# Kernel optimization log

Measured on AMD Instinct MI355X. Metric: run time of the kernel, lower is better.

## Reference

```python
import jax, jax.numpy as jnp
import numpy as np

N_NODES, IN_F, HIDDEN, N_EDGES, N_TRAIN, N_CLASS = 50000, 64, 512, 160000, 80000, 7
BN_EPS = 1e-5

def _lin(k, fin, fout):
    return jax.random.normal(k, (fin, fout), jnp.float32) * 0.05, jnp.zeros((fout,), jnp.float32)

def setup_inputs() -> dict:
    key = jax.random.key(0)
    ks = jax.random.split(key, 12)
    x = jax.random.normal(ks[0], (N_NODES, IN_F), jnp.float32)
    edge_index = jax.random.randint(ks[1], (2, N_EDGES), 0, N_NODES, jnp.int32)
    train_edge_id = jax.random.randint(ks[2], (N_TRAIN,), 0, N_EDGES, jnp.int32)
    W1, b1 = _lin(ks[3], IN_F, HIDDEN)
    W2, b2 = _lin(ks[4], HIDDEN, HIDDEN)
    W3, b3 = _lin(ks[5], HIDDEN, HIDDEN)
    W4, b4 = _lin(ks[6], HIDDEN, HIDDEN)
    lin1_W, lin1_b = _lin(ks[7], HIDDEN, HIDDEN)
    lin2_W, lin2_b = _lin(ks[8], HIDDEN, HIDDEN)
    fc2_W, fc2_b = _lin(ks[9], HIDDEN, N_CLASS)
    ones = jnp.ones((HIDDEN,), jnp.float32); zeros = jnp.zeros((HIDDEN,), jnp.float32)
    return dict(x=x, edge_index=edge_index, train_edge_id=train_edge_id,
                W1=W1, b1=b1, W2=W2, b2=b2, W3=W3, b3=b3,
                bn1_g=ones, bn1_b=zeros, bn1_m=zeros, bn1_v=ones, eps1=jnp.float32(0.0),
                W4=W4, b4=b4, bn2_g=ones, bn2_b=zeros, bn2_m=zeros, bn2_v=ones, eps2=jnp.float32(0.0),
                lin1_W=lin1_W, lin1_b=lin1_b, lin2_W=lin2_W, lin2_b=lin2_b,
                fc2_W=fc2_W, fc2_b=fc2_b)

def _gin_agg(h, src, dst, eps):
    # PyG GINConv: (1+eps)*x_i + sum_{j in N(i)} x_j, messages flow src->dst
    agg = jax.ops.segment_sum(h[src], dst, num_segments=N_NODES)
    return (1.0 + eps) * h + agg

def _bn(h, g, b, m, v):
    return (h - m) * jax.lax.rsqrt(v + BN_EPS) * g + b

def reference(x, edge_index, train_edge_id, W1, b1, W2, b2, W3, b3,
              bn1_g, bn1_b, bn1_m, bn1_v, eps1,
              W4, b4, bn2_g, bn2_b, bn2_m, bn2_v, eps2,
              lin1_W, lin1_b, lin2_W, lin2_b, fc2_W, fc2_b):
    src, dst = edge_index[0], edge_index[1]
    h = _gin_agg(x, src, dst, eps1)
    h = jax.nn.relu(h @ W1 + b1)
    h = jax.nn.relu(h @ W2 + b2)
    h = jax.nn.relu(h @ W3 + b3)
    h = _bn(h, bn1_g, bn1_b, bn1_m, bn1_v)
    # gin_convs[0]: agg -> Linear+ReLU -> BN
    h = _gin_agg(h, src, dst, eps2)
    h = jax.nn.relu(h @ W4 + b4)
    h = _bn(h, bn2_g, bn2_b, bn2_m, bn2_v)
    # node MLP head (dropout = identity in eval)
    h = jax.nn.relu(h @ lin1_W + lin1_b)
    h = h @ lin2_W + lin2_b
    # edge-gather fusion (feature_fusion=None -> elementwise mul)
    node_id = edge_index[:, train_edge_id]  # [2, T]
    x1 = h[node_id[0]]
    x2 = h[node_id[1]]
    return (x1 * x2) @ fc2_W + fc2_b  # [T, class_num]
```

## Files before the change

### kernel.cpp

```cpp
#include <hip/hip_runtime.h>

#define N_NODES 50000
#define MPAD    50048
#define IN_F    64
#define HIDDEN  512
#define N_EDGES 160000
#define N_TRAIN 80000
#define N_CLASS 7
#define BN_EPS  1e-5f

#define MT      (MPAD / 128)
#define NT      4
#define FULLGRP ((MT / 8) * 32)
#define NBLK    ((N_NODES + 255) / 256)

typedef short  bf16x8 __attribute__((ext_vector_type(8)));
typedef float  f32x4  __attribute__((ext_vector_type(4)));
typedef unsigned short ushort_t;

__device__ __forceinline__ ushort_t f2b(float v) {
    union { float f; unsigned int u; } c; c.f = v;
    unsigned int x = c.u;
    unsigned int r = (x + 0x7FFFu + ((x >> 16) & 1u)) >> 16;
    return (ushort_t)r;
}
__device__ __forceinline__ float b2f(ushort_t b) {
    union { unsigned int u; float f; } c; c.u = ((unsigned int)b) << 16;
    return c.f;
}

__device__ __forceinline__ void async_copy16(const void* g, void* l) {
    __builtin_amdgcn_global_load_lds(
        (const __attribute__((address_space(1))) void*)g,
        (__attribute__((address_space(3))) void*)l, 16, 0, 0);
}

__global__ void zero_kernel(int* __restrict__ p, int n) {
    int i = blockIdx.x * blockDim.x + threadIdx.x;
    if (i < n) p[i] = 0;
}

__global__ void hist_kernel(const int* __restrict__ ei, int* __restrict__ deg) {
    int e = blockIdx.x * blockDim.x + threadIdx.x;
    if (e >= N_EDGES) return;
    atomicAdd(&deg[ei[N_EDGES + e]], 1);
}

__global__ __launch_bounds__(256) void blocksum_kernel(const int* __restrict__ deg,
                                                       int* __restrict__ bsum) {
    __shared__ int s[256];
    int i = blockIdx.x * 256 + threadIdx.x;
    s[threadIdx.x] = (i < N_NODES) ? deg[i] : 0;
    __syncthreads();
    for (int off = 128; off > 0; off >>= 1) {
        if (threadIdx.x < off) s[threadIdx.x] += s[threadIdx.x + off];
        __syncthreads();
    }
    if (threadIdx.x == 0) bsum[blockIdx.x] = s[0];
}

__global__ __launch_bounds__(256) void scanbsum_kernel(const int* __restrict__ bsum,
                                                       int* __restrict__ boff) {
    __shared__ int s[256];
    int tid = threadIdx.x;
    s[tid] = (tid < NBLK) ? bsum[tid] : 0;
    __syncthreads();
    for (int off = 1; off < 256; off <<= 1) {
        int t = (tid >= off) ? s[tid - off] : 0;
        __syncthreads();
        s[tid] += t;
        __syncthreads();
    }
    if (tid < NBLK) boff[tid] = (tid == 0) ? 0 : s[tid - 1];
}

__global__ __launch_bounds__(256) void rowptr_kernel(const int* __restrict__ deg,
                                                     const int* __restrict__ boff,
                                                     int* __restrict__ rowptr,
                                                     int* __restrict__ cursor) {
    __shared__ int s[256];
    int tid = threadIdx.x;
    int i = blockIdx.x * 256 + tid;
    int d = (i < N_NODES) ? deg[i] : 0;
    s[tid] = d;
    __syncthreads();
    for (int off = 1; off < 256; off <<= 1) {
        int t = (tid >= off) ? s[tid - off] : 0;
        __syncthreads();
        s[tid] += t;
        __syncthreads();
    }
    int incl = s[tid] + boff[blockIdx.x];
    if (i < N_NODES) {
        rowptr[i + 1] = incl;
        cursor[i] = incl - d;
    }
    if (i == 0) rowptr[0] = 0;
}

__global__ void scatter_kernel(const int* __restrict__ ei,
                               int* __restrict__ cursor, int* __restrict__ adj) {
    int e = blockIdx.x * blockDim.x + threadIdx.x;
    if (e >= N_EDGES) return;
    int src = ei[e], dst = ei[N_EDGES + e];
    int pos = atomicAdd(&cursor[dst], 1);
    adj[pos] = src;
}

__global__ __launch_bounds__(256) void gather64_kernel(
    const float* __restrict__ x, const int* __restrict__ rowptr,
    const int* __restrict__ adj, const float* __restrict__ epsp,
    ushort_t* __restrict__ hi, ushort_t* __restrict__ lo) {
    int wave = threadIdx.x >> 6, lane = threadIdx.x & 63;
    int n = blockIdx.x * 4 + wave;
    if (n >= N_NODES) return;
    float s = 1.0f + *epsp;
    float sum = s * x[(size_t)n * IN_F + lane];
    int beg = rowptr[n], end = rowptr[n + 1];
    for (int k = beg; k < end; k++) {
        sum += x[(size_t)adj[k] * IN_F + lane];
    }
    ushort_t hb = f2b(sum);
    ushort_t lb = f2b(sum - b2f(hb));
    hi[(size_t)n * IN_F + lane] = hb;
    lo[(size_t)n * IN_F + lane] = lb;
}

__global__ __launch_bounds__(256) void gather512_kernel(
    const float* __restrict__ h, const int* __restrict__ rowptr,
    const int* __restrict__ adj, const float* __restrict__ epsp,
    ushort_t* __restrict__ hi, ushort_t* __restrict__ lo) {
    int wave = threadIdx.x >> 6, lane = threadIdx.x & 63;
    int n = blockIdx.x * 2 + (wave >> 1);
    if (n >= N_NODES) return;
    float s = 1.0f + *epsp;
    const int f = (wave & 1) * 256 + lane * 4;
    float4 a = *(const float4*)&h[(size_t)n * HIDDEN + f];
    float sum[4] = {s * a.x, s * a.y, s * a.z, s * a.w};
    int beg = rowptr[n], end = rowptr[n + 1];
    for (int k = beg; k < end; k++) {
        float4 b = *(const float4*)&h[(size_t)adj[k] * HIDDEN + f];
        sum[0] += b.x; sum[1] += b.y; sum[2] += b.z; sum[3] += b.w;
    }
    ushort_t h4[4], l4[4];
#pragma unroll
    for (int j = 0; j < 4; j++) {
        h4[j] = f2b(sum[j]);
        l4[j] = f2b(sum[j] - b2f(h4[j]));
    }
    *(ushort4*)&hi[(size_t)n * HIDDEN + f] = make_ushort4(h4[0], h4[1], h4[2], h4[3]);
    *(ushort4*)&lo[(size_t)n * HIDDEN + f] = make_ushort4(l4[0], l4[1], l4[2], l4[3]);
}

__global__ void wtrans_all_kernel(const float* __restrict__ w0,
                                  const float* __restrict__ w1,
                                  const float* __restrict__ w2,
                                  const float* __restrict__ w3,
                                  const float* __restrict__ w4,
                                  const float* __restrict__ w5,
                                  ushort_t* __restrict__ Wp) {
    const size_t WSMALL = (size_t)HIDDEN * IN_F;
    const size_t WBIG   = (size_t)HIDDEN * HIDDEN;
    int z = blockIdx.z;
    const float* W = (z == 0) ? w0 : (z == 1) ? w1 : (z == 2) ? w2
                   : (z == 3) ? w3 : (z == 4) ? w4 : w5;
    int K = (z == 0) ? IN_F : HIDDEN;
    size_t off_h = (z == 0) ? 0 : 2 * WSMALL + (size_t)(z - 1) * 2 * WBIG;
    ushort_t* Whi = Wp + off_h;
    ushort_t* Wlo = Whi + ((z == 0) ? WSMALL : WBIG);

    __shared__ float t[32][33];
    int tx = threadIdx.x & 31, ty = threadIdx.x >> 5;
    int nb = blockIdx.x * 32, kb = blockIdx.y * 32;
    if (kb >= K) return;
#pragma unroll
    for (int i = 0; i < 4; i++) {
        int k = kb + ty + i * 8;
        t[ty + i * 8][tx] = W[(size_t)k * HIDDEN + nb + tx];
    }
    __syncthreads();
#pragma unroll
    for (int i = 0; i < 4; i++) {
        int n = nb + ty + i * 8;
        int k = kb + tx;
        float v = t[tx][ty + i * 8];
        ushort_t hb = f2b(v);
        ushort_t lb = f2b(v - b2f(hb));
        Whi[(size_t)n * K + k] = hb;
        Wlo[(size_t)n * K + k] = lb;
    }
}

template<int K>
__global__ __launch_bounds__(256) void gemm_split_kernel(
    const ushort_t* __restrict__ Ahi, const ushort_t* __restrict__ Alo,
    const ushort_t* __restrict__ Bhi, const ushort_t* __restrict__ Blo,
    const float* __restrict__ bias,
    float* __restrict__ Cf, ushort_t* __restrict__ Chi, ushort_t* __restrict__ Clo,
    int mode,
    const float* __restrict__ bn_g, const float* __restrict__ bn_b,
    const float* __restrict__ bn_m, const float* __restrict__ bn_v) {
    __shared__ ushort_t As_h[2][128 * 32];
    __shared__ ushort_t As_l[2][128 * 32];
    __shared__ ushort_t Bs_h[2][128 * 32];
    __shared__ ushort_t Bs_l[2][128 * 32];

    const int tid  = threadIdx.x;
    const int wave = tid >> 6, lane = tid & 63;
    const int wm = wave >> 1, wn = wave & 1;
    const int quad = lane >> 4, r = lane & 15;

    int idx = blockIdx.x, m_t, n_t;
    if (idx < FULLGRP) {
        m_t = (idx >> 5) * 8 + (idx & 7);
        n_t = (idx >> 3) & 3;
    } else {
        int t = idx - FULLGRP;
        m_t = (FULLGRP >> 2) + (t >> 2);
        n_t = t & 3;
    }
    const int m0 = m_t * 128, n0 = n_t * 128;

    const f32x4 vzero = {0.f, 0.f, 0.f, 0.f};
    f32x4 acc[4][4];
#pragma unroll
    for (int i = 0; i < 4; i++)
#pragma unroll
        for (int j = 0; j < 4; j++) acc[i][j] = vzero;

    const int srow = lane >> 2;
    const int scol = (((lane & 3) + ((srow >> 1) & 3)) & 3) * 8;
    const int csw  = ((quad - ((r >> 1) & 3)) & 3) * 8;

    auto stage = [&](int k0, int b) {
#pragma unroll
        for (int tt = 0; tt < 2; tt++) {
            int rr = wave * 32 + tt * 16 + srow;
            int lbase = (wave * 32 + tt * 16) * 32;
            size_t ga = (size_t)(m0 + rr) * K + k0 + scol;
            size_t gb = (size_t)(n0 + rr) * K + k0 + scol;
            async_copy16(Ahi + ga, &As_h[b][lbase]);
            async_copy16(Alo + ga, &As_l[b][lbase]);
            async_copy16(Bhi + gb, &Bs_h[b][lbase]);
            async_copy16(Blo + gb, &Bs_l[b][lbase]);
        }
    };

    stage(0, 0);
    __syncthreads();

    for (int k0 = 0; k0 < K; k0 += 32) {
        const int cur = (k0 >> 5) & 1;
        if (k0 + 32 < K) stage(k0 + 32, cur ^ 1);

        bf16x8 ah[4], al[4], bh[4], bl[4];
#pragma unroll
        for (int i = 0; i < 4; i++) {
            int aofs = (wm * 64 + i * 16 + r) * 32 + csw;
            int bofs = (wn * 64 + i * 16 + r) * 32 + csw;
            ah[i] = *(const bf16x8*)&As_h[cur][aofs];
            al[i] = *(const bf16x8*)&As_l[cur][aofs];
            bh[i] = *(const bf16x8*)&Bs_h[cur][bofs];
            bl[i] = *(const bf16x8*)&Bs_l[cur][bofs];
        }
#pragma unroll
        for (int i = 0; i < 4; i++)
#pragma unroll
            for (int j = 0; j < 4; j++) {
                acc[i][j] = __builtin_amdgcn_mfma_f32_16x16x32_bf16(ah[i], bh[j], acc[i][j], 0, 0, 0);
                acc[i][j] = __builtin_amdgcn_mfma_f32_16x16x32_bf16(ah[i], bl[j], acc[i][j], 0, 0, 0);
                acc[i][j] = __builtin_amdgcn_mfma_f32_16x16x32_bf16(al[i], bh[j], acc[i][j], 0, 0, 0);
            }
        __syncthreads();
    }

    float bia[4], sc[4], sh[4];
#pragma unroll
    for (int j = 0; j < 4; j++) {
        int col = n0 + wn * 64 + j * 16 + r;
        bia[j] = bias[col];
        if (mode == 2) {
            float g = bn_g[col], bb = bn_b[col], mm = bn_m[col], vv = bn_v[col];
            sc[j] = g * rsqrtf(vv + BN_EPS);
            sh[j] = bb - mm * sc[j];
        } else { sc[j] = 1.f; sh[j] = 0.f; }
    }
#pragma unroll
    for (int i = 0; i < 4; i++) {
#pragma unroll
        for (int rg = 0; rg < 4; rg++) {
            int row = m0 + wm * 64 + i * 16 + quad * 4 + rg;
            if (row >= N_NODES) continue;
#pragma unroll
            for (int j = 0; j < 4; j++) {
                int col = n0 + wn * 64 + j * 16 + r;
                float v = acc[i][j][rg] + bia[j];
                if (mode >= 1) v = fmaxf(v, 0.f);
                if (mode == 2) v = v * sc[j] + sh[j];
                size_t oix = (size_t)row * HIDDEN + col;
                if (Cf) {
                    Cf[oix] = v;
                } else {
                    ushort_t hb = f2b(v);
                    ushort_t lb = f2b(v - b2f(hb));
                    Chi[oix] = hb;
                    Clo[oix] = lb;
                }
            }
        }
    }
}

__global__ __launch_bounds__(256) void gemm_k64_kernel(
    const ushort_t* __restrict__ Ahi, const ushort_t* __restrict__ Alo,
    const ushort_t* __restrict__ Bhi, const ushort_t* __restrict__ Blo,
    const float* __restrict__ bias,
    ushort_t* __restrict__ Chi, ushort_t* __restrict__ Clo) {
    const int K = 64;
    __shared__ ushort_t As_h[128 * 64];
    __shared__ ushort_t As_l[128 * 64];
    __shared__ ushort_t Bs_h[128 * 64];
    __shared__ ushort_t Bs_l[128 * 64];

    const int tid  = threadIdx.x;
    const int wave = tid >> 6, lane = tid & 63;
    const int wm = wave >> 1, wn = wave & 1;
    const int quad = lane >> 4, r = lane & 15;

    int idx = blockIdx.x, m_t, n_t;
    if (idx < FULLGRP) {
        m_t = (idx >> 5) * 8 + (idx & 7);
        n_t = (idx >> 3) & 3;
    } else {
        int t = idx - FULLGRP;
        m_t = (FULLGRP >> 2) + (t >> 2);
        n_t = t & 3;
    }
    const int m0 = m_t * 128, n0 = n_t * 128;

    const int srow8 = lane >> 3;
    const int sc8   = (((lane & 7) - srow8) & 7) * 8;
#pragma unroll
    for (int t = 0; t < 4; t++) {
        int base = wave * 32 + t * 8;
        int rr = base + srow8;
        int lbase = base * 64;
        size_t ga = (size_t)(m0 + rr) * K + sc8;
        size_t gb = (size_t)(n0 + rr) * K + sc8;
        async_copy16(Ahi + ga, &As_h[lbase]);
        async_copy16(Alo + ga, &As_l[lbase]);
        async_copy16(Bhi + gb, &Bs_h[lbase]);
        async_copy16(Blo + gb, &Bs_l[lbase]);
    }
    __syncthreads();

    const f32x4 vzero = {0.f, 0.f, 0.f, 0.f};
    f32x4 acc[4][4];
#pragma unroll
    for (int i = 0; i < 4; i++)
#pragma unroll
        for (int j = 0; j < 4; j++) acc[i][j] = vzero;

#pragma unroll
    for (int ks = 0; ks < 2; ks++) {
        bf16x8 ah[4], al[4], bh[4], bl[4];
#pragma unroll
        for (int i = 0; i < 4; i++) {
            int ra = wm * 64 + i * 16 + r;
            int rb = wn * 64 + i * 16 + r;
            int ca = ((quad + ks * 4 + (ra & 7)) & 7) * 8;
            int cb = ((quad + ks * 4 + (rb & 7)) & 7) * 8;
            ah[i] = *(const bf16x8*)&As_h[ra * 64 + ca];
            al[i] = *(const bf16x8*)&As_l[ra * 64 + ca];
            bh[i] = *(const bf16x8*)&Bs_h[rb * 64 + cb];
            bl[i] = *(const bf16x8*)&Bs_l[rb * 64 + cb];
        }
#pragma unroll
        for (int i = 0; i < 4; i++)
#pragma unroll
            for (int j = 0; j < 4; j++) {
                acc[i][j] = __builtin_amdgcn_mfma_f32_16x16x32_bf16(ah[i], bh[j], acc[i][j], 0, 0, 0);
                acc[i][j] = __builtin_amdgcn_mfma_f32_16x16x32_bf16(ah[i], bl[j], acc[i][j], 0, 0, 0);
                acc[i][j] = __builtin_amdgcn_mfma_f32_16x16x32_bf16(al[i], bh[j], acc[i][j], 0, 0, 0);
            }
    }

    float bia[4];
#pragma unroll
    for (int j = 0; j < 4; j++) bia[j] = bias[n0 + wn * 64 + j * 16 + r];
#pragma unroll
    for (int i = 0; i < 4; i++) {
#pragma unroll
        for (int rg = 0; rg < 4; rg++) {
            int row = m0 + wm * 64 + i * 16 + quad * 4 + rg;
            if (row >= N_NODES) continue;
#pragma unroll
            for (int j = 0; j < 4; j++) {
                int col = n0 + wn * 64 + j * 16 + r;
                float v = fmaxf(acc[i][j][rg] + bia[j], 0.f);
                size_t oix = (size_t)row * HIDDEN + col;
                ushort_t hb = f2b(v);
                ushort_t lb = f2b(v - b2f(hb));
                Chi[oix] = hb;
                Clo[oix] = lb;
            }
        }
    }
}

__global__ __launch_bounds__(256) void fc2_kernel(
    const float* __restrict__ h, const int* __restrict__ ei,
    const int* __restrict__ teid, const float* __restrict__ W,
    const float* __restrict__ bias, float* __restrict__ out) {
    __shared__ float Ws[HIDDEN * N_CLASS];
    __shared__ float bs[N_CLASS];
    for (int i = threadIdx.x; i < HIDDEN * N_CLASS; i += blockDim.x) Ws[i] = W[i];
    if (threadIdx.x < N_CLASS) bs[threadIdx.x] = bias[threadIdx.x];
    __syncthreads();

    int wave = threadIdx.x >> 6;
    int lane = threadIdx.x & 63;
    int t = blockIdx.x * 4 + wave;
    if (t >= N_TRAIN) return;

    int e = teid[t];
    int a = ei[e];
    int b = ei[N_EDGES + e];
    const float* xa = h + (size_t)a * HIDDEN;
    const float* xb = h + (size_t)b * HIDDEN;

    float acc[N_CLASS];
#pragma unroll
    for (int c = 0; c < N_CLASS; c++) acc[c] = 0.f;

    int j0 = lane * 8;
    float4 a0 = *(const float4*)&xa[j0];
    float4 a1 = *(const float4*)&xa[j0 + 4];
    float4 b0 = *(const float4*)&xb[j0];
    float4 b1 = *(const float4*)&xb[j0 + 4];
    float p[8] = {a0.x * b0.x, a0.y * b0.y, a0.z * b0.z, a0.w * b0.w,
                  a1.x * b1.x, a1.y * b1.y, a1.z * b1.z, a1.w * b1.w};
#pragma unroll
    for (int jj = 0; jj < 8; jj++) {
        const float* wrow = &Ws[(j0 + jj) * N_CLASS];
#pragma unroll
        for (int c = 0; c < N_CLASS; c++) acc[c] = fmaf(p[jj], wrow[c], acc[c]);
    }
#pragma unroll
    for (int c = 0; c < N_CLASS; c++) {
        float v = acc[c];
        for (int off = 32; off > 0; off >>= 1) v += __shfl_down(v, off, 64);
        if (lane == 0) out[(size_t)t * N_CLASS + c] = v + bs[c];
    }
}

extern "C" void kernel_launch(void* const* d_in, const int* in_sizes, int n_in,
                              void* d_out, int out_size, void* d_ws, size_t ws_size,
                              hipStream_t stream) {
    const float* x      = (const float*)d_in[0];
    const int*   ei     = (const int*)d_in[1];
    const int*   teid   = (const int*)d_in[2];
    const float* W1     = (const float*)d_in[3];
    const float* b1     = (const float*)d_in[4];
    const float* W2     = (const float*)d_in[5];
    const float* b2     = (const float*)d_in[6];
    const float* W3     = (const float*)d_in[7];
    const float* b3     = (const float*)d_in[8];
    const float* bn1_g  = (const float*)d_in[9];
    const float* bn1_b  = (const float*)d_in[10];
    const float* bn1_m  = (const float*)d_in[11];
    const float* bn1_v  = (const float*)d_in[12];
    const float* eps1   = (const float*)d_in[13];
    const float* W4     = (const float*)d_in[14];
    const float* b4     = (const float*)d_in[15];
    const float* bn2_g  = (const float*)d_in[16];
    const float* bn2_b  = (const float*)d_in[17];
    const float* bn2_m  = (const float*)d_in[18];
    const float* bn2_v  = (const float*)d_in[19];
    const float* eps2   = (const float*)d_in[20];
    const float* lin1_W = (const float*)d_in[21];
    const float* lin1_b = (const float*)d_in[22];
    const float* lin2_W = (const float*)d_in[23];
    const float* lin2_b = (const float*)d_in[24];
    const float* fc2_W  = (const float*)d_in[25];
    const float* fc2_b  = (const float*)d_in[26];

    const size_t PLANE   = (size_t)MPAD * HIDDEN;
    const size_t PLANE64 = (size_t)MPAD * IN_F;

    ushort_t* R0h = (ushort_t*)d_ws;
    ushort_t* R0l = R0h + PLANE;
    ushort_t* R1h = R0l + PLANE;
    ushort_t* R1l = R1h + PLANE;

    const size_t WSMALL = (size_t)HIDDEN * IN_F;
    const size_t WBIG   = (size_t)HIDDEN * HIDDEN;
    ushort_t* Wp   = R1l + PLANE;
    ushort_t* Wt1h = Wp;            ushort_t* Wt1l = Wt1h + WSMALL;
    ushort_t* Wt2h = Wt1l + WSMALL; ushort_t* Wt2l = Wt2h + WBIG;
    ushort_t* Wt3h = Wt2l + WBIG;   ushort_t* Wt3l = Wt3h + WBIG;
    ushort_t* Wt4h = Wt3l + WBIG;   ushort_t* Wt4l = Wt4h + WBIG;
    ushort_t* Wt5h = Wt4l + WBIG;   ushort_t* Wt5l = Wt5h + WBIG;
    ushort_t* Wt6h = Wt5l + WBIG;   ushort_t* Wt6l = Wt6h + WBIG;

    int* deg    = (int*)(Wt6l + WBIG);
    int* cursor = deg + N_NODES;
    int* rowptr = cursor + N_NODES;
    int* bsum   = rowptr + (N_NODES + 1);
    int* boff   = bsum + NBLK;
    int* adj    = boff + NBLK;

    float* F32_R0 = (float*)R0h;
    ushort_t* H0h = R1h;
    ushort_t* H0l = R1h + PLANE64;

    zero_kernel<<<(N_NODES + 255) / 256, 256, 0, stream>>>(deg, N_NODES);
    hist_kernel<<<(N_EDGES + 255) / 256, 256, 0, stream>>>(ei, deg);
    blocksum_kernel<<<NBLK, 256, 0, stream>>>(deg, bsum);
    scanbsum_kernel<<<1, 256, 0, stream>>>(bsum, boff);
    rowptr_kernel<<<NBLK, 256, 0, stream>>>(deg, boff, rowptr, cursor);
    scatter_kernel<<<(N_EDGES + 255) / 256, 256, 0, stream>>>(ei, cursor, adj);

    wtrans_all_kernel<<<dim3(16, 16, 6), 256, 0, stream>>>(W1, W2, W3, W4,
                                                           lin1_W, lin2_W, Wp);

    const int ngrid = MT * NT;
    int nwb = (N_NODES + 3) / 4;

    gather64_kernel<<<nwb, 256, 0, stream>>>(x, rowptr, adj, eps1, H0h, H0l);

    gemm_k64_kernel<<<ngrid, 256, 0, stream>>>(H0h, H0l, Wt1h, Wt1l, b1, R0h, R0l);
    gemm_split_kernel<HIDDEN><<<ngrid, 256, 0, stream>>>(R0h, R0l, Wt2h, Wt2l, b2,
        nullptr, R1h, R1l, 1, nullptr, nullptr, nullptr, nullptr);
    gemm_split_kernel<HIDDEN><<<ngrid, 256, 0, stream>>>(R1h, R1l, Wt3h, Wt3l, b3,
        F32_R0, nullptr, nullptr, 2, bn1_g, bn1_b, bn1_m, bn1_v);

    gather512_kernel<<<(N_NODES + 1) / 2, 256, 0, stream>>>(F32_R0, rowptr, adj,
                                                            eps2, R1h, R1l);

    gemm_split_kernel<HIDDEN><<<ngrid, 256, 0, stream>>>(R1h, R1l, Wt4h, Wt4l, b4,
        nullptr, R0h, R0l, 2, bn2_g, bn2_b, bn2_m, bn2_v);
    gemm_split_kernel<HIDDEN><<<ngrid, 256, 0, stream>>>(R0h, R0l, Wt5h, Wt5l, lin1_b,
        nullptr, R1h, R1l, 1, nullptr, nullptr, nullptr, nullptr);
    gemm_split_kernel<HIDDEN><<<ngrid, 256, 0, stream>>>(R1h, R1l, Wt6h, Wt6l, lin2_b,
        F32_R0, nullptr, nullptr, 0, nullptr, nullptr, nullptr, nullptr);

    fc2_kernel<<<(N_TRAIN + 3) / 4, 256, 0, stream>>>(F32_R0, ei, teid, fc2_W, fc2_b,
                                                      (float*)d_out);
}
```

Measured before the change: 914.4 us.

## Use 256x128 tiles with triple-buffered async pipeline in split-bf16 GEMMs

Replaces the 128x128, 256-thread split-bf16 GEMM with a 512-thread kernel that computes 256x128 output tiles. Operands are staged through a three-deep LDS ring, using explicit vmcnt waits and a single barrier per K-step instead of two syncthreads. The hi/lo fragment loads are interleaved with the three MFMA passes, and setprio raises wave priority around MFMA bursts. The goals are more reuse of B tiles, better latency hiding and fewer synchronisation stalls. The cost is about 147KB of LDS per block, which limits occupancy, and the last M tile reads rows past MPAD.

Result: slower. 968.5 us (+5.9%).

```diff
diff --git a/kernel.cpp b/kernel.cpp
--- a/kernel.cpp
+++ b/kernel.cpp
@@ -13,6 +13,10 @@
 #define NT      4
 #define FULLGRP ((MT / 8) * 32)
 #define NBLK    ((N_NODES + 255) / 256)
+
+#define MT2     ((MPAD + 255) / 256)
+#define FULLG2  ((MT2 / 8) * 32)
+#define NG2     (MT2 * 4)
 
 typedef short  bf16x8 __attribute__((ext_vector_type(8)));
 typedef float  f32x4  __attribute__((ext_vector_type(4)));
@@ -191,8 +195,7 @@
     }
 }
 
-template<int K>
-__global__ __launch_bounds__(256) void gemm_split_kernel(
+__global__ __launch_bounds__(512, 2) void gemm_split8_kernel(
     const ushort_t* __restrict__ Ahi, const ushort_t* __restrict__ Alo,
     const ushort_t* __restrict__ Bhi, const ushort_t* __restrict__ Blo,
     const float* __restrict__ bias,
@@ -200,10 +203,11 @@
     int mode,
     const float* __restrict__ bn_g, const float* __restrict__ bn_b,
     const float* __restrict__ bn_m, const float* __restrict__ bn_v) {
-    __shared__ ushort_t As_h[2][128 * 32];
-    __shared__ ushort_t As_l[2][128 * 32];
-    __shared__ ushort_t Bs_h[2][128 * 32];
-    __shared__ ushort_t Bs_l[2][128 * 32];
+    const int K = HIDDEN;
+    __shared__ ushort_t As_h[3][256 * 32];
+    __shared__ ushort_t As_l[3][256 * 32];
+    __shared__ ushort_t Bs_h[3][128 * 32];
+    __shared__ ushort_t Bs_l[3][128 * 32];
 
     const int tid  = threadIdx.x;
     const int wave = tid >> 6, lane = tid & 63;
@@ -211,15 +215,15 @@
     const int quad = lane >> 4, r = lane & 15;
 
     int idx = blockIdx.x, m_t, n_t;
-    if (idx < FULLGRP) {
+    if (idx < FULLG2) {
         m_t = (idx >> 5) * 8 + (idx & 7);
         n_t = (idx >> 3) & 3;
     } else {
-        int t = idx - FULLGRP;
-        m_t = (FULLGRP >> 2) + (t >> 2);
-        n_t = t & 3;
-    }
-    const int m0 = m_t * 128, n0 = n_t * 128;
+        int t2 = idx - FULLG2;
+        m_t = (FULLG2 >> 2) + (t2 >> 2);
+        n_t = t2 & 3;
+    }
+    const int m0 = m_t * 256, n0 = n_t * 128;
 
     const f32x4 vzero = {0.f, 0.f, 0.f, 0.f};
     f32x4 acc[4][4];
@@ -232,46 +236,83 @@
     const int scol = (((lane & 3) + ((srow >> 1) & 3)) & 3) * 8;
     const int csw  = ((quad - ((r >> 1) & 3)) & 3) * 8;
 
-    auto stage = [&](int k0, int b) {
+    auto stage = [&](int kt, int b) {
+        const int k0 = kt * 32;
 #pragma unroll
         for (int tt = 0; tt < 2; tt++) {
-            int rr = wave * 32 + tt * 16 + srow;
-            int lbase = (wave * 32 + tt * 16) * 32;
-            size_t ga = (size_t)(m0 + rr) * K + k0 + scol;
-            size_t gb = (size_t)(n0 + rr) * K + k0 + scol;
-            async_copy16(Ahi + ga, &As_h[b][lbase]);
-            async_copy16(Alo + ga, &As_l[b][lbase]);
-            async_copy16(Bhi + gb, &Bs_h[b][lbase]);
-            async_copy16(Blo + gb, &Bs_l[b][lbase]);
+            int rra = wave * 32 + tt * 16 + srow;
+            int lba = (wave * 32 + tt * 16) * 32;
+            size_t ga = (size_t)(m0 + rra) * K + k0 + scol;
+            async_copy16(Ahi + ga, &As_h[b][lba]);
+            async_copy16(Alo + ga, &As_l[b][lba]);
+        }
+        {
+            int rrb = wave * 16 + srow;
+            int lbb = (wave * 16) * 32;
+            size_t gb = (size_t)(n0 + rrb) * K + k0 + scol;
+            async_copy16(Bhi + gb, &Bs_h[b][lbb]);
+            async_copy16(Blo + gb, &Bs_l[b][lbb]);
         }
     };
 
     stage(0, 0);
-    __syncthreads();
-
-    for (int k0 = 0; k0 < K; k0 += 32) {
-        const int cur = (k0 >> 5) & 1;
-        if (k0 + 32 < K) stage(k0 + 32, cur ^ 1);
-
-        bf16x8 ah[4], al[4], bh[4], bl[4];
+    stage(1, 1);
+    asm volatile("s_waitcnt vmcnt(6)" ::: "memory");
+    __builtin_amdgcn_s_barrier();
+
+#pragma unroll
+    for (int t = 0; t < 16; t++) {
+        const int cur = t % 3;
+        if (t + 2 < 16) stage(t + 2, (t + 2) % 3);
+
+        bf16x8 ah[4], bh[4], al[4], bl[4];
 #pragma unroll
         for (int i = 0; i < 4; i++) {
             int aofs = (wm * 64 + i * 16 + r) * 32 + csw;
-            int bofs = (wn * 64 + i * 16 + r) * 32 + csw;
             ah[i] = *(const bf16x8*)&As_h[cur][aofs];
+        }
+#pragma unroll
+        for (int j = 0; j < 4; j++) {
+            int bofs = (wn * 64 + j * 16 + r) * 32 + csw;
+            bh[j] = *(const bf16x8*)&Bs_h[cur][bofs];
+        }
+        __builtin_amdgcn_s_setprio(1);
+#pragma unroll
+        for (int i = 0; i < 4; i++)
+#pragma unroll
+            for (int j = 0; j < 4; j++)
+                acc[i][j] = __builtin_amdgcn_mfma_f32_16x16x32_bf16(ah[i], bh[j], acc[i][j], 0, 0, 0);
+        __builtin_amdgcn_s_setprio(0);
+#pragma unroll
+        for (int j = 0; j < 4; j++) {
+            int bofs = (wn * 64 + j * 16 + r) * 32 + csw;
+            bl[j] = *(const bf16x8*)&Bs_l[cur][bofs];
+        }
+        __builtin_amdgcn_s_setprio(1);
+#pragma unroll
+        for (int i = 0; i < 4; i++)
+#pragma unroll
+            for (int j = 0; j < 4; j++)
+                acc[i][j] = __builtin_amdgcn_mfma_f32_16x16x32_bf16(ah[i], bl[j], acc[i][j], 0, 0, 0);
+        __builtin_amdgcn_s_setprio(0);
+#pragma unroll
+        for (int i = 0; i < 4; i++) {
+            int aofs = (wm * 64 + i * 16 + r) * 32 + csw;
             al[i] = *(const bf16x8*)&As_l[cur][aofs];
-            bh[i] = *(const bf16x8*)&Bs_h[cur][bofs];
-            bl[i] = *(const bf16x8*)&Bs_l[cur][bofs];
-        }
+        }
+        __builtin_amdgcn_s_setprio(1);
 #pragma unroll
         for (int i = 0; i < 4; i++)
 #pragma unroll
-            for (int j = 0; j < 4; j++) {
-                acc[i][j] = __builtin_amdgcn_mfma_f32_16x16x32_bf16(ah[i], bh[j], acc[i][j], 0, 0, 0);
-                acc[i][j] = __builtin_amdgcn_mfma_f32_16x16x32_bf16(ah[i], bl[j], acc[i][j], 0, 0, 0);
+            for (int j = 0; j < 4; j++)
                 acc[i][j] = __builtin_amdgcn_mfma_f32_16x16x32_bf16(al[i], bh[j], acc[i][j], 0, 0, 0);
-            }
-        __syncthreads();
+        __builtin_amdgcn_s_setprio(0);
+
+        if (t < 15) {
+            if (t < 14) asm volatile("s_waitcnt vmcnt(6)" ::: "memory");
+            else        asm volatile("s_waitcnt vmcnt(0)" ::: "memory");
+            __builtin_amdgcn_s_barrier();
+        }
     }
 
     float bia[4], sc[4], sh[4];
@@ -530,19 +571,19 @@
     gather64_kernel<<<nwb, 256, 0, stream>>>(x, rowptr, adj, eps1, H0h, H0l);
 
     gemm_k64_kernel<<<ngrid, 256, 0, stream>>>(H0h, H0l, Wt1h, Wt1l, b1, R0h, R0l);
-    gemm_split_kernel<HIDDEN><<<ngrid, 256, 0, stream>>>(R0h, R0l, Wt2h, Wt2l, b2,
+    gemm_split8_kernel<<<NG2, 512, 0, stream>>>(R0h, R0l, Wt2h, Wt2l, b2,
         nullptr, R1h, R1l, 1, nullptr, nullptr, nullptr, nullptr);
-    gemm_split_kernel<HIDDEN><<<ngrid, 256, 0, stream>>>(R1h, R1l, Wt3h, Wt3l, b3,
+    gemm_split8_kernel<<<NG2, 512, 0, stream>>>(R1h, R1l, Wt3h, Wt3l, b3,
         F32_R0, nullptr, nullptr, 2, bn1_g, bn1_b, bn1_m, bn1_v);
 
     gather512_kernel<<<(N_NODES + 1) / 2, 256, 0, stream>>>(F32_R0, rowptr, adj,
                                                             eps2, R1h, R1l);
 
-    gemm_split_kernel<HIDDEN><<<ngrid, 256, 0, stream>>>(R1h, R1l, Wt4h, Wt4l, b4,
+    gemm_split8_kernel<<<NG2, 512, 0, stream>>>(R1h, R1l, Wt4h, Wt4l, b4,
         nullptr, R0h, R0l, 2, bn2_g, bn2_b, bn2_m, bn2_v);
-    gemm_split_kernel<HIDDEN><<<ngrid, 256, 0, stream>>>(R0h, R0l, Wt5h, Wt5l, lin1_b,
+    gemm_split8_kernel<<<NG2, 512, 0, stream>>>(R0h, R0l, Wt5h, Wt5l, lin1_b,
         nullptr, R1h, R1l, 1, nullptr, nullptr, nullptr, nullptr);
-    gemm_split_kernel<HIDDEN><<<ngrid, 256, 0, stream>>>(R1h, R1l, Wt6h, Wt6l, lin2_b,
+    gemm_split8_kernel<<<NG2, 512, 0, stream>>>(R1h, R1l, Wt6h, Wt6l, lin2_b,
         F32_R0, nullptr, nullptr, 0, nullptr, nullptr, nullptr, nullptr);
 
     fc2_kernel<<<(N_TRAIN + 3) / 4, 256, 0, stream>>>(F32_R0, ei, teid, fc2_W, fc2_b,
```
